# Performance work log

Hardware: AMD Instinct MI355X
Metric: run time of the kernel (lower is better)

Reference implementation:

```python
import jax, jax.numpy as jnp
import numpy as np

N_TABLES = 26
ROWS = 100001   # n + 1 per EmbeddingBag
D = 64          # m_spa
B = 8192
L = 4           # fixed pooling factor per bag


def setup_inputs() -> dict:
    key = jax.random.key(0)
    ks = jax.random.split(key, 16)
    inp = {}
    inp["dense_x"] = jax.random.normal(ks[0], (B, 13), dtype=jnp.float32)
    # offsets: bag k starts at k*L (fixed pooling factor), same for every table
    inp["lS_o"] = jnp.tile(jnp.arange(B, dtype=jnp.int64) * L, (N_TABLES, 1))
    inp["lS_i"] = jax.random.randint(ks[1], (N_TABLES, B * L), 0, 100000).astype(jnp.int64)
    # embedding tables, uniform(-r, r) with r = sqrt(2/(n+m))
    r = (2.0 / (100000 + D)) ** 0.5
    inp["emb_tables"] = jax.random.uniform(ks[2], (N_TABLES, ROWS, D), dtype=jnp.float32, minval=-r, maxval=r)
    def lin(k, n_in, n_out):
        k1, k2 = jax.random.split(k)
        w = jax.random.normal(k1, (n_out, n_in), dtype=jnp.float32) * (2.0 / n_in) ** 0.5
        b = jax.random.uniform(k2, (n_out,), dtype=jnp.float32, minval=-n_in**-0.5, maxval=n_in**-0.5)
        return w, b
    inp["bot_w0"], inp["bot_b0"] = lin(ks[3], 13, 512)
    inp["bot_w1"], inp["bot_b1"] = lin(ks[4], 512, 256)
    inp["bot_w2"], inp["bot_b2"] = lin(ks[5], 256, 64)
    inp["top_w0"], inp["top_b0"] = lin(ks[6], 415, 512)
    inp["top_w1"], inp["top_b1"] = lin(ks[7], 512, 256)
    inp["top_w2"], inp["top_b2"] = lin(ks[8], 256, 1)
    return inp


def _dlrm(dense_x, lS_o, lS_i, emb_tables,
          bot_w0, bot_b0, bot_w1, bot_b1, bot_w2, bot_b2,
          top_w0, top_b0, top_w1, top_b1, top_w2, top_b2):
    # bottom MLP: Linear+ReLU for every layer (sigmoid_bot=-1)
    x = jax.nn.relu(dense_x @ bot_w0.T + bot_b0)
    x = jax.nn.relu(x @ bot_w1.T + bot_b1)
    x = jax.nn.relu(x @ bot_w2.T + bot_b2)          # [B, D]
    # EmbeddingBag mean pooling per table (fixed bag length L encoded by lS_o)
    idx = lS_i.reshape(N_TABLES, B, L)
    gathered = jax.vmap(lambda tab, ix: tab[ix])(emb_tables, idx)  # [T, B, L, D]
    ly = gathered.mean(axis=2)                       # [T, B, D]
    # dot interaction: T_feat = cat([x]+ly) -> [B, 27, D]
    T_feat = jnp.concatenate([x[None], ly], axis=0).transpose(1, 0, 2)
    Z = jnp.einsum('bnd,bmd->bnm', T_feat, T_feat)   # [B, 27, 27]
    li, lj = np.tril_indices(N_TABLES + 1, -1)       # strict lower triangle (offset=0)
    Zflat = Z[:, li, lj]                             # [B, 351]
    R = jnp.concatenate([x, Zflat], axis=1)          # [B, 415]
    # top MLP: sigmoid_top=2 -> loop breaks before appending Sigmoid -> last layer linear
    z = jax.nn.relu(R @ top_w0.T + top_b0)
    z = jax.nn.relu(z @ top_w1.T + top_b1)
    z = z @ top_w2.T + top_b2                        # [B, 1]
    return z.reshape(-1)


def reference(dense_x, lS_o, lS_i, emb_tables,
              bot_w0, bot_b0, bot_w1, bot_b1, bot_w2, bot_b2,
              top_w0, top_b0, top_w1, top_b1, top_w2, top_b2):
    return _dlrm(dense_x, lS_o, lS_i, emb_tables,
                 bot_w0, bot_b0, bot_w1, bot_b1, bot_w2, bot_b2,
                 top_w0, top_b0, top_w1, top_b1, top_w2, top_b2)
```

## Files before the change

### kernel.cpp

```cpp
#include <hip/hip_runtime.h>
#include <hip/hip_bf16.h>

typedef short bf16x8 __attribute__((ext_vector_type(8)));
typedef float f32x4 __attribute__((ext_vector_type(4)));

__device__ __forceinline__ float relu_f(float v){ return v > 0.f ? v : 0.f; }

__device__ __forceinline__ f32x4 mfma16(bf16x8 a, bf16x8 b, f32x4 c){
  return __builtin_amdgcn_mfma_f32_16x16x32_bf16(a, b, c, 0, 0, 0);
}

__device__ __forceinline__ short bfbits(float v){
  __hip_bfloat16 h = __float2bfloat16(v);
  return *reinterpret_cast<short*>(&h);
}

__global__ __launch_bounds__(256) void prep(
    const float* __restrict__ X,  const float* __restrict__ bw0,
    const float* __restrict__ bb0, __hip_bfloat16* __restrict__ H,
    const float* __restrict__ bw1, __hip_bfloat16* __restrict__ w1b,
    const float* __restrict__ bw2, __hip_bfloat16* __restrict__ w2b,
    const float* __restrict__ tw0, __hip_bfloat16* __restrict__ tw0b,
    const float* __restrict__ tw1, __hip_bfloat16* __restrict__ tw1b){
  int blk = blockIdx.x;
  if (blk < 512){
    int n = threadIdx.x;
    int m0 = blk * 16;
    float w0[13], w1[13];
#pragma unroll
    for (int k = 0; k < 13; k++){ w0[k] = bw0[n*13 + k]; w1[k] = bw0[(n+256)*13 + k]; }
    float b0 = bb0[n], b1 = bb0[n + 256];
    for (int mi = 0; mi < 16; mi++){
      int m = m0 + mi;
      float a0 = b0, a1 = b1;
#pragma unroll
      for (int k = 0; k < 13; k++){
        float xv = X[m*13 + k];
        a0 += xv * w0[k]; a1 += xv * w1[k];
      }
      H[(size_t)m*512 + n]       = __float2bfloat16(relu_f(a0));
      H[(size_t)m*512 + n + 256] = __float2bfloat16(relu_f(a1));
    }
  } else if (blk < 1024){
    int i = (blk - 512)*256 + threadIdx.x;
    w1b[i] = __float2bfloat16(bw1[i]);
  } else if (blk < 1088){
    int i = (blk - 1024)*256 + threadIdx.x;
    w2b[i] = __float2bfloat16(bw2[i]);
  } else if (blk < 1920){
    int i = (blk - 1088)*256 + threadIdx.x;
    int r = i / 416, k = i - r*416;
    float v = (k < 415) ? tw0[r*415 + k] : 0.f;
    tw0b[i] = __float2bfloat16(v);
  } else {
    int i = (blk - 1920)*256 + threadIdx.x;
    tw1b[i] = __float2bfloat16(tw1[i]);
  }
}

template<int NT, int K>
__global__ __launch_bounds__(256) void gemm_br(const __hip_bfloat16* __restrict__ A,
    const __hip_bfloat16* __restrict__ W, const float* __restrict__ Bv,
    __hip_bfloat16* __restrict__ C, int N, int ldc){
  int lane = threadIdx.x & 63;
  int wave = blockIdx.x * 4 + (threadIdx.x >> 6);
  int ntiles = N / (16 * NT);
  int mi = wave / ntiles, ni = wave % ntiles;
  int row = lane & 15, quad = lane >> 4;
  const __hip_bfloat16* Ap = A + (size_t)(mi*16 + row) * K + quad*8;
  const __hip_bfloat16* Wp = W + (size_t)(ni*16*NT + row) * K + quad*8;
  f32x4 acc[NT];
#pragma unroll
  for (int t = 0; t < NT; t++) acc[t] = (f32x4){0.f, 0.f, 0.f, 0.f};
#pragma unroll
  for (int k = 0; k < K; k += 32){
    bf16x8 a = *(const bf16x8*)(Ap + k);
#pragma unroll
    for (int t = 0; t < NT; t++){
      bf16x8 b = *(const bf16x8*)(Wp + (size_t)t*16*K + k);
      acc[t] = mfma16(a, b, acc[t]);
    }
  }
#pragma unroll
  for (int t = 0; t < NT; t++){
    int n = ni*16*NT + t*16 + row;
    float bn = Bv[n];
#pragma unroll
    for (int r = 0; r < 4; r++){
      int m = mi*16 + quad*4 + r;
      C[(size_t)m*ldc + n] = __float2bfloat16(relu_f(acc[t][r] + bn));
    }
  }
}

__global__ __launch_bounds__(256) void embint(const int* __restrict__ I,
    const float* __restrict__ T, __hip_bfloat16* __restrict__ R){
  __shared__ __align__(16) float ly[4][26][68];
  int wv   = threadIdx.x >> 6;
  int lane = threadIdx.x & 63;
  int b    = blockIdx.x * 4 + wv;
  float (*L)[68] = ly[wv];

  int4 myix = (int4){0,0,0,0};
  if (lane < 26) myix = *(const int4*)(I + ((size_t)lane << 15) + (b << 2));

#pragma unroll
  for (int t = 0; t < 26; t++){
    int i0 = __builtin_amdgcn_readlane(myix.x, t);
    int i1 = __builtin_amdgcn_readlane(myix.y, t);
    int i2 = __builtin_amdgcn_readlane(myix.z, t);
    int i3 = __builtin_amdgcn_readlane(myix.w, t);
    const float* tb = T + (size_t)t * 6400064ull + lane;
    float s0 = tb[(size_t)(unsigned)i0 * 64];
    float s1 = tb[(size_t)(unsigned)i1 * 64];
    float s2 = tb[(size_t)(unsigned)i2 * 64];
    float s3 = tb[(size_t)(unsigned)i3 * 64];
    L[t][lane] = (((s0 + s1) + s2) + s3) * 0.25f;
  }
  __syncthreads();

  int row = lane & 15, quad = lane >> 4;
  __hip_bfloat16* Rb = R + (size_t)b * 416;

  f32x4 a00 = {0,0,0,0}, a10 = {0,0,0,0}, a11 = {0,0,0,0};
#pragma unroll
  for (int k = 0; k < 64; k += 32){
    int ko = k + quad*8;
    bf16x8 f0, f1 = {0,0,0,0,0,0,0,0};
    if (row == 0){
      f0 = *(const bf16x8*)(Rb + ko);
    } else {
      const float* p = L[row - 1] + ko;
#pragma unroll
      for (int j = 0; j < 8; j++) f0[j] = bfbits(p[j]);
    }
    if (row < 11){
      const float* p = L[row + 15] + ko;
#pragma unroll
      for (int j = 0; j < 8; j++) f1[j] = bfbits(p[j]);
    }
    a00 = mfma16(f0, f0, a00);
    a10 = mfma16(f1, f0, a10);
    a11 = mfma16(f1, f1, a11);
  }
#pragma unroll
  for (int r = 0; r < 4; r++){
    { int i = quad*4 + r, j = row;
      if (i > j) Rb[64 + i*(i-1)/2 + j] = __float2bfloat16(a00[r]); }
    { int i = 16 + quad*4 + r, j = row;
      if (i < 27) Rb[64 + i*(i-1)/2 + j] = __float2bfloat16(a10[r]); }
    { int i = 16 + quad*4 + r, j = 16 + row;
      if (i < 27 && i > j) Rb[64 + i*(i-1)/2 + j] = __float2bfloat16(a11[r]); }
  }
  if (lane == 0) Rb[415] = __float2bfloat16(0.f);
}

template<int K>
__global__ __launch_bounds__(256) void top12(const __hip_bfloat16* __restrict__ A,
    const __hip_bfloat16* __restrict__ W, const float* __restrict__ Bv,
    const float* __restrict__ W2, const float* __restrict__ b2,
    float* __restrict__ O){
  __shared__ float part[4][16];
  int lane = threadIdx.x & 63, wv = threadIdx.x >> 6;
  int mi = blockIdx.x;
  int row = lane & 15, quad = lane >> 4;
  const __hip_bfloat16* Ap = A + (size_t)(mi*16 + row) * K + quad*8;
  int nb = wv * 64;
  const __hip_bfloat16* Wp = W + (size_t)(nb + row) * K + quad*8;
  f32x4 acc[4];
#pragma unroll
  for (int t = 0; t < 4; t++) acc[t] = (f32x4){0.f, 0.f, 0.f, 0.f};
#pragma unroll
  for (int k = 0; k < K; k += 32){
    bf16x8 a = *(const bf16x8*)(Ap + k);
#pragma unroll
    for (int t = 0; t < 4; t++){
      bf16x8 b = *(const bf16x8*)(Wp + (size_t)t*16*K + k);
      acc[t] = mfma16(a, b, acc[t]);
    }
  }
  float p[4];
#pragma unroll
  for (int r = 0; r < 4; r++){
    float s = 0.f;
#pragma unroll
    for (int t = 0; t < 4; t++){
      int n = nb + t*16 + row;
      s += relu_f(acc[t][r] + Bv[n]) * W2[n];
    }
    p[r] = s;
  }
#pragma unroll
  for (int r = 0; r < 4; r++){
#pragma unroll
    for (int o = 1; o < 16; o <<= 1) p[r] += __shfl_xor(p[r], o, 64);
  }
  if (row == 0){
#pragma unroll
    for (int r = 0; r < 4; r++) part[wv][quad*4 + r] = p[r];
  }
  __syncthreads();
  if (threadIdx.x < 16){
    float s = part[0][threadIdx.x] + part[1][threadIdx.x]
            + part[2][threadIdx.x] + part[3][threadIdx.x] + b2[0];
    O[mi*16 + threadIdx.x] = s;
  }
}

extern "C" void kernel_launch(void* const* d_in, const int* in_sizes, int n_in,
                              void* d_out, int out_size, void* d_ws, size_t ws_size,
                              hipStream_t stream) {
  const float* dense_x = (const float*)d_in[0];
  const int*   lS_i    = (const int*)d_in[2];
  const float* tables  = (const float*)d_in[3];
  const float* bw0 = (const float*)d_in[4];  const float* bb0 = (const float*)d_in[5];
  const float* bw1 = (const float*)d_in[6];  const float* bb1 = (const float*)d_in[7];
  const float* bw2 = (const float*)d_in[8];  const float* bb2 = (const float*)d_in[9];
  const float* tw0 = (const float*)d_in[10]; const float* tb0 = (const float*)d_in[11];
  const float* tw1 = (const float*)d_in[12]; const float* tb1 = (const float*)d_in[13];
  const float* tw2 = (const float*)d_in[14]; const float* tb2 = (const float*)d_in[15];
  float* out = (float*)d_out;
  char* ws = (char*)d_ws;

  __hip_bfloat16* w1b  = (__hip_bfloat16*)(ws + 0);
  __hip_bfloat16* w2b  = (__hip_bfloat16*)(ws + 262144);
  __hip_bfloat16* tw0b = (__hip_bfloat16*)(ws + 294912);
  __hip_bfloat16* tw1b = (__hip_bfloat16*)(ws + 720896);
  __hip_bfloat16* h0   = (__hip_bfloat16*)(ws + 983040);
  __hip_bfloat16* h1   = (__hip_bfloat16*)(ws + 9371648);
  __hip_bfloat16* R    = (__hip_bfloat16*)(ws + 13565952);
  __hip_bfloat16* h3   = h0;

  prep<<<2432, 256, 0, stream>>>(dense_x, bw0, bb0, h0,
                                 bw1, w1b, bw2, w2b, tw0, tw0b, tw1, tw1b);
  gemm_br<4,512><<<512, 256, 0, stream>>>(h0, w1b, bb1, h1, 256, 256);
  gemm_br<1,256><<<512, 256, 0, stream>>>(h1, w2b, bb2, R, 64, 416);
  embint<<<8192/4, 256, 0, stream>>>(lS_i, tables, R);
  gemm_br<4,416><<<1024, 256, 0, stream>>>(R, tw0b, tb0, h3, 512, 512);
  top12<512><<<512, 256, 0, stream>>>(h3, tw1b, tb1, tw2, tb2, out);

  (void)in_sizes; (void)n_in; (void)out_size; (void)ws_size;
}
```

Before: 848.8 us.

## Fuse bottom MLP layers 0 and 1, keeping layer-0 activations in shared memory

The first bottom-MLP layer is computed into a shared-memory tile, and the second layer's MFMA GEMM runs in the same kernel. Layer-1 weights are read as fp32 and converted to bf16 on the fly. This removes the h0 global round trip, the separate bw1 conversion pass and one kernel launch. In exchange, every block rereads and reconverts the full fp32 layer-1 weight matrix, which doubles the weight bytes fetched per block.

```diff
diff --git a/kernel.cpp b/kernel.cpp
--- a/kernel.cpp
+++ b/kernel.cpp
@@ -15,15 +15,32 @@
   return *reinterpret_cast<short*>(&h);
 }
 
-__global__ __launch_bounds__(256) void prep(
+__global__ __launch_bounds__(256) void botl01(
     const float* __restrict__ X,  const float* __restrict__ bw0,
-    const float* __restrict__ bb0, __hip_bfloat16* __restrict__ H,
-    const float* __restrict__ bw1, __hip_bfloat16* __restrict__ w1b,
+    const float* __restrict__ bb0,
+    const float* __restrict__ bw1, const float* __restrict__ bb1,
+    __hip_bfloat16* __restrict__ h1,
     const float* __restrict__ bw2, __hip_bfloat16* __restrict__ w2b,
     const float* __restrict__ tw0, __hip_bfloat16* __restrict__ tw0b,
     const float* __restrict__ tw1, __hip_bfloat16* __restrict__ tw1b){
   int blk = blockIdx.x;
-  if (blk < 512){
+  if (blk >= 512){
+    if (blk < 576){
+      int i = (blk - 512)*256 + threadIdx.x;
+      w2b[i] = __float2bfloat16(bw2[i]);
+    } else if (blk < 1408){
+      int i = (blk - 576)*256 + threadIdx.x;
+      int r = i / 416, k = i - r*416;
+      float v = (k < 415) ? tw0[r*415 + k] : 0.f;
+      tw0b[i] = __float2bfloat16(v);
+    } else {
+      int i = (blk - 1408)*256 + threadIdx.x;
+      tw1b[i] = __float2bfloat16(tw1[i]);
+    }
+    return;
+  }
+  __shared__ __hip_bfloat16 hs[16][520];
+  {
     int n = threadIdx.x;
     int m0 = blk * 16;
     float w0[13], w1[13];
@@ -38,23 +55,39 @@
         float xv = X[m*13 + k];
         a0 += xv * w0[k]; a1 += xv * w1[k];
       }
-      H[(size_t)m*512 + n]       = __float2bfloat16(relu_f(a0));
-      H[(size_t)m*512 + n + 256] = __float2bfloat16(relu_f(a1));
-    }
-  } else if (blk < 1024){
-    int i = (blk - 512)*256 + threadIdx.x;
-    w1b[i] = __float2bfloat16(bw1[i]);
-  } else if (blk < 1088){
-    int i = (blk - 1024)*256 + threadIdx.x;
-    w2b[i] = __float2bfloat16(bw2[i]);
-  } else if (blk < 1920){
-    int i = (blk - 1088)*256 + threadIdx.x;
-    int r = i / 416, k = i - r*416;
-    float v = (k < 415) ? tw0[r*415 + k] : 0.f;
-    tw0b[i] = __float2bfloat16(v);
-  } else {
-    int i = (blk - 1920)*256 + threadIdx.x;
-    tw1b[i] = __float2bfloat16(tw1[i]);
+      hs[mi][n]       = __float2bfloat16(relu_f(a0));
+      hs[mi][n + 256] = __float2bfloat16(relu_f(a1));
+    }
+  }
+  __syncthreads();
+  int lane = threadIdx.x & 63;
+  int ni   = threadIdx.x >> 6;
+  int row = lane & 15, quad = lane >> 4;
+  const float* Wp = bw1 + (size_t)(ni*64 + row) * 512 + quad*8;
+  f32x4 acc[4];
+#pragma unroll
+  for (int t = 0; t < 4; t++) acc[t] = (f32x4){0.f, 0.f, 0.f, 0.f};
+#pragma unroll
+  for (int k = 0; k < 512; k += 32){
+    bf16x8 a = *(const bf16x8*)&hs[row][quad*8 + k];
+#pragma unroll
+    for (int t = 0; t < 4; t++){
+      const float* wp = Wp + (size_t)t*16*512 + k;
+      bf16x8 b;
+#pragma unroll
+      for (int j = 0; j < 8; j++) b[j] = bfbits(wp[j]);
+      acc[t] = mfma16(a, b, acc[t]);
+    }
+  }
+#pragma unroll
+  for (int t = 0; t < 4; t++){
+    int n = ni*64 + t*16 + row;
+    float bn = bb1[n];
+#pragma unroll
+    for (int r = 0; r < 4; r++){
+      int m = blk*16 + quad*4 + r;
+      h1[(size_t)m*256 + n] = __float2bfloat16(relu_f(acc[t][r] + bn));
+    }
   }
 }
 
@@ -222,18 +255,15 @@
   float* out = (float*)d_out;
   char* ws = (char*)d_ws;
 
-  __hip_bfloat16* w1b  = (__hip_bfloat16*)(ws + 0);
   __hip_bfloat16* w2b  = (__hip_bfloat16*)(ws + 262144);
   __hip_bfloat16* tw0b = (__hip_bfloat16*)(ws + 294912);
   __hip_bfloat16* tw1b = (__hip_bfloat16*)(ws + 720896);
-  __hip_bfloat16* h0   = (__hip_bfloat16*)(ws + 983040);
+  __hip_bfloat16* h3   = (__hip_bfloat16*)(ws + 983040);
   __hip_bfloat16* h1   = (__hip_bfloat16*)(ws + 9371648);
   __hip_bfloat16* R    = (__hip_bfloat16*)(ws + 13565952);
-  __hip_bfloat16* h3   = h0;
-
-  prep<<<2432, 256, 0, stream>>>(dense_x, bw0, bb0, h0,
-                                 bw1, w1b, bw2, w2b, tw0, tw0b, tw1, tw1b);
-  gemm_br<4,512><<<512, 256, 0, stream>>>(h0, w1b, bb1, h1, 256, 256);
+
+  botl01<<<1920, 256, 0, stream>>>(dense_x, bw0, bb0, bw1, bb1, h1,
+                                   bw2, w2b, tw0, tw0b, tw1, tw1b);
   gemm_br<1,256><<<512, 256, 0, stream>>>(h1, w2b, bb2, R, 64, 416);
   embint<<<8192/4, 256, 0, stream>>>(lS_i, tables, R);
   gemm_br<4,416><<<1024, 256, 0, stream>>>(R, tw0b, tb0, h3, 512, 512);
```

Result: no change. 855.4 us (+0.8%).
